# Optimization experiments

Measured on AMD Instinct MI355X. Metric: run time of the kernel, lower is better.

Reference implementation:

```python
import jax, jax.numpy as jnp
import numpy as np

D, B, E, O = 16, 8, 2048, 2048  # delays, batch, pre, post


def setup_inputs() -> dict:
    key = jax.random.key(0)
    k1, k2, k3, k4, k5, k6 = jax.random.split(key, 6)
    # Sparse nonnegative connectivity scaled by wmax (here wmax=1)
    conn = (jax.random.uniform(k1, (E, O)) < 0.2).astype(jnp.float32)
    W = jax.random.uniform(k2, (E, O), dtype=jnp.float32) * conn
    # align_signs: per-presynaptic-neuron sign in {-1,+1}, zeroed where W<=0
    signs_pre = jnp.where(jax.random.uniform(k3, (E,)) < 0.8, 1.0, -1.0)
    signs = jnp.where(W > 0, signs_pre[:, None], 0.0).astype(jnp.float32)
    Xd = (jax.random.uniform(k4, (D, B, E)) < 0.05).astype(jnp.float32)
    # STP module output (before the +1 applied in forward)
    Wshort = 0.1 * jax.random.normal(k5, (D, B, E), dtype=jnp.float32)
    # delaymap: binary routing mask (delay, pre, post)
    delaymap = (jax.random.uniform(k6, (D, E, O)) < 0.3).astype(jnp.float32)
    return {"W": W, "signs": signs, "Xd": Xd, "Wshort": Wshort, "delaymap": delaymap}


def reference(W, signs, Xd, Wshort, delaymap):
    # DeltaSynapse.forward, active, has_STDP=False, has_STP=True:
    #   W_eff = signs * W                      (e, o)
    #   Wshort_mod = shortterm(Xd) + 1         (d, b, e)
    #   I = einsum('eo,dbe,deo,dbe->bo', W_eff, Xd, delaymap, Wshort_mod)
    Weff = signs * W
    I = jnp.einsum('eo,dbe,deo,dbe->bo', Weff, Xd, delaymap, Wshort + 1.0)
    return I
```

## Files before the change

kernel.cpp:

```cpp
#include <hip/hip_runtime.h>
#include <cstdint>
#include <cstddef>

#define DD 16
#define BB 8
#define EE 2048
#define OO 2048
#define NCH 128

__global__ void pack_coeffs(const float* __restrict__ Xd,
                            const float* __restrict__ Ws,
                            float* __restrict__ Cpack,
                            float* __restrict__ out) {
    int i = blockIdx.x * 256 + threadIdx.x;
    if (i < BB * OO) out[i] = 0.0f;
    if (i >= DD * BB * EE) return;
    int e  = i & (EE - 1);
    int db = i >> 11;
    int d  = db >> 3;
    int b  = db & 7;
    float x = Xd[i];
    Cpack[(size_t)e * (DD * BB) + d * BB + b] = x * (Ws[i] + 1.0f);
}

__device__ __forceinline__ void fma4(float4& a, const float4& x, float s) {
    a.x = fmaf(x.x, s, a.x);
    a.y = fmaf(x.y, s, a.y);
    a.z = fmaf(x.z, s, a.z);
    a.w = fmaf(x.w, s, a.w);
}

__global__ __launch_bounds__(256, 4)
void synapse_main(const float* __restrict__ W,
                  const float* __restrict__ S,
                  const float* __restrict__ DM,
                  const float* __restrict__ Cpack,
                  float* __restrict__ out) {
    const int ot    = blockIdx.x;
    const int ch    = blockIdx.y;
    const int wave  = threadIdx.x >> 6;
    const int lane  = threadIdx.x & 63;
    const int o0    = ot * 256 + lane * 4;
    const int ebase = ch * 16 + wave * 4;

    const int q_ln = lane >> 4;
    const int d_ln = lane & 15;
    const float4* crow = reinterpret_cast<const float4*>(
        Cpack + ((size_t)(ebase + q_ln) * (DD * BB)) + d_ln * BB);
    float4 ca = crow[0];
    float4 cb = crow[1];
    bool nz = (ca.x != 0.f) | (ca.y != 0.f) | (ca.z != 0.f) | (ca.w != 0.f) |
              (cb.x != 0.f) | (cb.y != 0.f) | (cb.z != 0.f) | (cb.w != 0.f);
    unsigned long long bal = __ballot(nz);
    unsigned m[4];
#pragma unroll
    for (int q = 0; q < 4; ++q) m[q] = (unsigned)(bal >> (16 * q)) & 0xFFFFu;

    float4 wf[4];
#pragma unroll
    for (int q = 0; q < 4; ++q) {
        float4 w4 = *reinterpret_cast<const float4*>(W + (size_t)(ebase + q) * OO + o0);
        float4 s4 = *reinterpret_cast<const float4*>(S + (size_t)(ebase + q) * OO + o0);
        wf[q].x = w4.x * s4.x; wf[q].y = w4.y * s4.y;
        wf[q].z = w4.z * s4.z; wf[q].w = w4.w * s4.w;
    }

    float4 acc[BB];
#pragma unroll
    for (int b = 0; b < BB; ++b) acc[b] = make_float4(0.f, 0.f, 0.f, 0.f);

    while (m[0] | m[1] | m[2] | m[3]) {
        float4 dmv[4];
        int    dsrc[4];
        unsigned act = 0;
#pragma unroll
        for (int q = 0; q < 4; ++q) {
            if (m[q]) {
                const int d = __builtin_ctz(m[q]);
                m[q] &= (m[q] - 1);
                dsrc[q] = q * 16 + d;
                dmv[q] = *reinterpret_cast<const float4*>(
                    DM + ((size_t)d * EE + (ebase + q)) * OO + o0);
                act |= 1u << q;
            }
        }
#pragma unroll
        for (int q = 0; q < 4; ++q) {
            if (act & (1u << q)) {
                const int sl = dsrc[q];
                float4 dw;
                dw.x = dmv[q].x * wf[q].x; dw.y = dmv[q].y * wf[q].y;
                dw.z = dmv[q].z * wf[q].z; dw.w = dmv[q].w * wf[q].w;
                fma4(acc[0], dw, __shfl(ca.x, sl));
                fma4(acc[1], dw, __shfl(ca.y, sl));
                fma4(acc[2], dw, __shfl(ca.z, sl));
                fma4(acc[3], dw, __shfl(ca.w, sl));
                fma4(acc[4], dw, __shfl(cb.x, sl));
                fma4(acc[5], dw, __shfl(cb.y, sl));
                fma4(acc[6], dw, __shfl(cb.z, sl));
                fma4(acc[7], dw, __shfl(cb.w, sl));
            }
        }
    }

    __shared__ __align__(16) float red[4][4][256];
    const int t = threadIdx.x;
#pragma unroll
    for (int p = 0; p < 2; ++p) {
#pragma unroll
        for (int bb = 0; bb < 4; ++bb)
            *reinterpret_cast<float4*>(&red[wave][bb][lane * 4]) = acc[p * 4 + bb];
        __syncthreads();
#pragma unroll
        for (int bb = 0; bb < 4; ++bb) {
            float s = red[0][bb][t] + red[1][bb][t] +
                      red[2][bb][t] + red[3][bb][t];
            atomicAdd(out + (size_t)(p * 4 + bb) * OO + ot * 256 + t, s);
        }
        __syncthreads();
    }
}

__global__ __launch_bounds__(256, 4)
void synapse_nows(const float* __restrict__ W,
                  const float* __restrict__ S,
                  const float* __restrict__ Xd,
                  const float* __restrict__ Ws,
                  const float* __restrict__ DM,
                  float* __restrict__ out) {
    const int ot    = blockIdx.x;
    const int ch    = blockIdx.y;
    const int wave  = threadIdx.x >> 6;
    const int lane  = threadIdx.x & 63;
    const int o0    = ot * 256 + lane * 4;
    const int ebase = ch * 16 + wave * 4;

    float4 acc[BB];
#pragma unroll
    for (int b = 0; b < BB; ++b) acc[b] = make_float4(0.f, 0.f, 0.f, 0.f);

    for (int ei = 0; ei < 4; ++ei) {
        const int e = ebase + ei;
        float4 w4 = *reinterpret_cast<const float4*>(W + (size_t)e * OO + o0);
        float4 s4 = *reinterpret_cast<const float4*>(S + (size_t)e * OO + o0);
        float4 wf;
        wf.x = w4.x * s4.x; wf.y = w4.y * s4.y;
        wf.z = w4.z * s4.z; wf.w = w4.w * s4.w;

        for (int d = 0; d < DD; ++d) {
            float c[BB];
            bool nz = false;
#pragma unroll
            for (int b = 0; b < BB; ++b) {
                size_t idx = (size_t)(d * BB + b) * EE + e;
                float x = Xd[idx];
                c[b] = x * (Ws[idx] + 1.0f);
                nz |= (c[b] != 0.f);
            }
            if (!nz) continue;
            float4 dm = *reinterpret_cast<const float4*>(
                DM + ((size_t)d * EE + e) * OO + o0);
            float4 dw;
            dw.x = dm.x * wf.x; dw.y = dm.y * wf.y;
            dw.z = dm.z * wf.z; dw.w = dm.w * wf.w;
#pragma unroll
            for (int b = 0; b < BB; ++b) fma4(acc[b], dw, c[b]);
        }
    }

    __shared__ __align__(16) float red[4][4][256];
    const int t = threadIdx.x;
#pragma unroll
    for (int p = 0; p < 2; ++p) {
#pragma unroll
        for (int bb = 0; bb < 4; ++bb)
            *reinterpret_cast<float4*>(&red[wave][bb][lane * 4]) = acc[p * 4 + bb];
        __syncthreads();
#pragma unroll
        for (int bb = 0; bb < 4; ++bb) {
            float s = red[0][bb][t] + red[1][bb][t] +
                      red[2][bb][t] + red[3][bb][t];
            atomicAdd(out + (size_t)(p * 4 + bb) * OO + ot * 256 + t, s);
        }
        __syncthreads();
    }
}

__global__ void zero_out(float* __restrict__ out) {
    int i = blockIdx.x * 256 + threadIdx.x;
    if (i < BB * OO) out[i] = 0.0f;
}

extern "C" void kernel_launch(void* const* d_in, const int* in_sizes, int n_in,
                              void* d_out, int out_size, void* d_ws, size_t ws_size,
                              hipStream_t stream) {
    const float* W  = (const float*)d_in[0];
    const float* S  = (const float*)d_in[1];
    const float* Xd = (const float*)d_in[2];
    const float* Ws = (const float*)d_in[3];
    const float* DM = (const float*)d_in[4];
    float* out = (float*)d_out;

    const size_t packBytes = (size_t)EE * DD * BB * sizeof(float);

    dim3 grid(8, NCH), blk(256);

    if (ws_size >= packBytes) {
        float* Cp = (float*)d_ws;
        pack_coeffs<<<(DD * BB * EE + 255) / 256, 256, 0, stream>>>(Xd, Ws, Cp, out);
        synapse_main<<<grid, blk, 0, stream>>>(W, S, DM, Cp, out);
    } else {
        zero_out<<<(BB * OO + 255) / 256, 256, 0, stream>>>(out);
        synapse_nows<<<grid, blk, 0, stream>>>(W, S, Xd, Ws, DM, out);
    }
}
```

Measured before the change: 349.3 us.

## Compact active (delay, pre) pairs into a global list and stream-partition them

```diff
diff --git a/kernel.cpp b/kernel.cpp
--- a/kernel.cpp
+++ b/kernel.cpp
@@ -6,13 +6,16 @@
 #define BB 8
 #define EE 2048
 #define OO 2048
-#define NCH 128
-
-__global__ void pack_coeffs(const float* __restrict__ Xd,
-                            const float* __restrict__ Ws,
-                            float* __restrict__ Cpack,
-                            float* __restrict__ out) {
+#define MAXP (EE * DD)
+#define NPART 256
+
+__global__ void prep(const float* __restrict__ Xd,
+                     const float* __restrict__ Ws,
+                     float* __restrict__ Cpack,
+                     unsigned* __restrict__ counter,
+                     float* __restrict__ out) {
     int i = blockIdx.x * 256 + threadIdx.x;
+    if (i == 0) *counter = 0;
     if (i < BB * OO) out[i] = 0.0f;
     if (i >= DD * BB * EE) return;
     int e  = i & (EE - 1);
@@ -23,6 +26,49 @@
     Cpack[(size_t)e * (DD * BB) + d * BB + b] = x * (Ws[i] + 1.0f);
 }
 
+__global__ void build_list(const float* __restrict__ Cpack,
+                           unsigned* __restrict__ counter,
+                           uint2* __restrict__ meta,
+                           float4* __restrict__ coef) {
+    const int t = threadIdx.x;
+    const int e = blockIdx.x * 256 + t;
+
+    unsigned msk = 0;
+    const float4* row = reinterpret_cast<const float4*>(Cpack + (size_t)e * (DD * BB));
+    for (int d = 0; d < DD; ++d) {
+        float4 a = row[d * 2];
+        float4 b = row[d * 2 + 1];
+        bool nz = (a.x != 0.f) | (a.y != 0.f) | (a.z != 0.f) | (a.w != 0.f) |
+                  (b.x != 0.f) | (b.y != 0.f) | (b.z != 0.f) | (b.w != 0.f);
+        msk |= (nz ? 1u : 0u) << d;
+    }
+    unsigned cnt = __popc(msk);
+
+    __shared__ unsigned sc[256];
+    __shared__ unsigned gbase;
+    sc[t] = cnt;
+    __syncthreads();
+    for (int off = 1; off < 256; off <<= 1) {
+        unsigned v = (t >= off) ? sc[t - off] : 0;
+        __syncthreads();
+        sc[t] += v;
+        __syncthreads();
+    }
+    if (t == 255) gbase = atomicAdd(counter, sc[255]);
+    __syncthreads();
+
+    unsigned ofs = gbase + sc[t] - cnt;
+    unsigned mm = msk;
+    while (mm) {
+        const int d = __builtin_ctz(mm);
+        mm &= (mm - 1);
+        meta[ofs] = make_uint2((unsigned)(d * EE + e), (unsigned)e);
+        coef[ofs * 2]     = row[d * 2];
+        coef[ofs * 2 + 1] = row[d * 2 + 1];
+        ++ofs;
+    }
+}
+
 __device__ __forceinline__ void fma4(float4& a, const float4& x, float s) {
     a.x = fmaf(x.x, s, a.x);
     a.y = fmaf(x.y, s, a.y);
@@ -30,95 +76,82 @@
     a.w = fmaf(x.w, s, a.w);
 }
 
-__global__ __launch_bounds__(256, 4)
-void synapse_main(const float* __restrict__ W,
-                  const float* __restrict__ S,
-                  const float* __restrict__ DM,
-                  const float* __restrict__ Cpack,
-                  float* __restrict__ out) {
-    const int ot    = blockIdx.x;
-    const int ch    = blockIdx.y;
-    const int wave  = threadIdx.x >> 6;
-    const int lane  = threadIdx.x & 63;
-    const int o0    = ot * 256 + lane * 4;
-    const int ebase = ch * 16 + wave * 4;
-
-    const int q_ln = lane >> 4;
-    const int d_ln = lane & 15;
-    const float4* crow = reinterpret_cast<const float4*>(
-        Cpack + ((size_t)(ebase + q_ln) * (DD * BB)) + d_ln * BB);
-    float4 ca = crow[0];
-    float4 cb = crow[1];
-    bool nz = (ca.x != 0.f) | (ca.y != 0.f) | (ca.z != 0.f) | (ca.w != 0.f) |
-              (cb.x != 0.f) | (cb.y != 0.f) | (cb.z != 0.f) | (cb.w != 0.f);
-    unsigned long long bal = __ballot(nz);
-    unsigned m[4];
-#pragma unroll
-    for (int q = 0; q < 4; ++q) m[q] = (unsigned)(bal >> (16 * q)) & 0xFFFFu;
-
-    float4 wf[4];
-#pragma unroll
-    for (int q = 0; q < 4; ++q) {
-        float4 w4 = *reinterpret_cast<const float4*>(W + (size_t)(ebase + q) * OO + o0);
-        float4 s4 = *reinterpret_cast<const float4*>(S + (size_t)(ebase + q) * OO + o0);
-        wf[q].x = w4.x * s4.x; wf[q].y = w4.y * s4.y;
-        wf[q].z = w4.z * s4.z; wf[q].w = w4.w * s4.w;
-    }
+__global__ __launch_bounds__(256, 2)
+void synapse_stream(const float* __restrict__ W,
+                    const float* __restrict__ S,
+                    const float* __restrict__ DM,
+                    const unsigned* __restrict__ counter,
+                    const uint2* __restrict__ meta,
+                    const float4* __restrict__ coef,
+                    float* __restrict__ out) {
+    const int o0 = blockIdx.y * 1024 + threadIdx.x * 4;
+    const unsigned P = *counter;
+    const int chunk = (int)((P + NPART - 1) / NPART);
+    int p  = blockIdx.x * chunk;
+    int p1 = p + chunk;
+    if (p1 > (int)P) p1 = (int)P;
 
     float4 acc[BB];
 #pragma unroll
     for (int b = 0; b < BB; ++b) acc[b] = make_float4(0.f, 0.f, 0.f, 0.f);
 
-    while (m[0] | m[1] | m[2] | m[3]) {
-        float4 dmv[4];
-        int    dsrc[4];
-        unsigned act = 0;
-#pragma unroll
-        for (int q = 0; q < 4; ++q) {
-            if (m[q]) {
-                const int d = __builtin_ctz(m[q]);
-                m[q] &= (m[q] - 1);
-                dsrc[q] = q * 16 + d;
-                dmv[q] = *reinterpret_cast<const float4*>(
-                    DM + ((size_t)d * EE + (ebase + q)) * OO + o0);
-                act |= 1u << q;
-            }
-        }
-#pragma unroll
-        for (int q = 0; q < 4; ++q) {
-            if (act & (1u << q)) {
-                const int sl = dsrc[q];
-                float4 dw;
-                dw.x = dmv[q].x * wf[q].x; dw.y = dmv[q].y * wf[q].y;
-                dw.z = dmv[q].z * wf[q].z; dw.w = dmv[q].w * wf[q].w;
-                fma4(acc[0], dw, __shfl(ca.x, sl));
-                fma4(acc[1], dw, __shfl(ca.y, sl));
-                fma4(acc[2], dw, __shfl(ca.z, sl));
-                fma4(acc[3], dw, __shfl(ca.w, sl));
-                fma4(acc[4], dw, __shfl(cb.x, sl));
-                fma4(acc[5], dw, __shfl(cb.y, sl));
-                fma4(acc[6], dw, __shfl(cb.z, sl));
-                fma4(acc[7], dw, __shfl(cb.w, sl));
-            }
-        }
-    }
-
-    __shared__ __align__(16) float red[4][4][256];
-    const int t = threadIdx.x;
-#pragma unroll
-    for (int p = 0; p < 2; ++p) {
-#pragma unroll
-        for (int bb = 0; bb < 4; ++bb)
-            *reinterpret_cast<float4*>(&red[wave][bb][lane * 4]) = acc[p * 4 + bb];
-        __syncthreads();
-#pragma unroll
-        for (int bb = 0; bb < 4; ++bb) {
-            float s = red[0][bb][t] + red[1][bb][t] +
-                      red[2][bb][t] + red[3][bb][t];
-            atomicAdd(out + (size_t)(p * 4 + bb) * OO + ot * 256 + t, s);
-        }
-        __syncthreads();
-    }
+    for (; p + 4 <= p1; p += 4) {
+        uint2  mv[4];
+        float4 dm[4], w4[4], s4[4];
+#pragma unroll
+        for (int j = 0; j < 4; ++j) mv[j] = meta[p + j];
+#pragma unroll
+        for (int j = 0; j < 4; ++j) {
+            dm[j] = *reinterpret_cast<const float4*>(DM + (size_t)mv[j].x * OO + o0);
+            w4[j] = *reinterpret_cast<const float4*>(W  + (size_t)mv[j].y * OO + o0);
+            s4[j] = *reinterpret_cast<const float4*>(S  + (size_t)mv[j].y * OO + o0);
+        }
+#pragma unroll
+        for (int j = 0; j < 4; ++j) {
+            float4 c0 = coef[(size_t)(p + j) * 2];
+            float4 c1 = coef[(size_t)(p + j) * 2 + 1];
+            float4 dw;
+            dw.x = dm[j].x * w4[j].x * s4[j].x;
+            dw.y = dm[j].y * w4[j].y * s4[j].y;
+            dw.z = dm[j].z * w4[j].z * s4[j].z;
+            dw.w = dm[j].w * w4[j].w * s4[j].w;
+            fma4(acc[0], dw, c0.x); fma4(acc[1], dw, c0.y);
+            fma4(acc[2], dw, c0.z); fma4(acc[3], dw, c0.w);
+            fma4(acc[4], dw, c1.x); fma4(acc[5], dw, c1.y);
+            fma4(acc[6], dw, c1.z); fma4(acc[7], dw, c1.w);
+        }
+    }
+    for (; p < p1; ++p) {
+        uint2 mv = meta[p];
+        float4 dm = *reinterpret_cast<const float4*>(DM + (size_t)mv.x * OO + o0);
+        float4 w4 = *reinterpret_cast<const float4*>(W  + (size_t)mv.y * OO + o0);
+        float4 s4 = *reinterpret_cast<const float4*>(S  + (size_t)mv.y * OO + o0);
+        float4 c0 = coef[(size_t)p * 2];
+        float4 c1 = coef[(size_t)p * 2 + 1];
+        float4 dw;
+        dw.x = dm.x * w4.x * s4.x;
+        dw.y = dm.y * w4.y * s4.y;
+        dw.z = dm.z * w4.z * s4.z;
+        dw.w = dm.w * w4.w * s4.w;
+        fma4(acc[0], dw, c0.x); fma4(acc[1], dw, c0.y);
+        fma4(acc[2], dw, c0.z); fma4(acc[3], dw, c0.w);
+        fma4(acc[4], dw, c1.x); fma4(acc[5], dw, c1.y);
+        fma4(acc[6], dw, c1.z); fma4(acc[7], dw, c1.w);
+    }
+
+#pragma unroll
+    for (int b = 0; b < BB; ++b) {
+        float* op = out + (size_t)b * OO + o0;
+        atomicAdd(op + 0, acc[b].x);
+        atomicAdd(op + 1, acc[b].y);
+        atomicAdd(op + 2, acc[b].z);
+        atomicAdd(op + 3, acc[b].w);
+    }
+}
+
+__global__ void zero_out(float* __restrict__ out) {
+    int i = blockIdx.x * 256 + threadIdx.x;
+    if (i < BB * OO) out[i] = 0.0f;
 }
 
 __global__ __launch_bounds__(256, 4)
@@ -171,24 +204,19 @@
     __shared__ __align__(16) float red[4][4][256];
     const int t = threadIdx.x;
 #pragma unroll
-    for (int p = 0; p < 2; ++p) {
+    for (int pp = 0; pp < 2; ++pp) {
 #pragma unroll
         for (int bb = 0; bb < 4; ++bb)
-            *reinterpret_cast<float4*>(&red[wave][bb][lane * 4]) = acc[p * 4 + bb];
+            *reinterpret_cast<float4*>(&red[wave][bb][lane * 4]) = acc[pp * 4 + bb];
         __syncthreads();
 #pragma unroll
         for (int bb = 0; bb < 4; ++bb) {
             float s = red[0][bb][t] + red[1][bb][t] +
                       red[2][bb][t] + red[3][bb][t];
-            atomicAdd(out + (size_t)(p * 4 + bb) * OO + ot * 256 + t, s);
-        }
-        __syncthreads();
-    }
-}
-
-__global__ void zero_out(float* __restrict__ out) {
-    int i = blockIdx.x * 256 + threadIdx.x;
-    if (i < BB * OO) out[i] = 0.0f;
+            atomicAdd(out + (size_t)(pp * 4 + bb) * OO + ot * 256 + t, s);
+        }
+        __syncthreads();
+    }
 }
 
 extern "C" void kernel_launch(void* const* d_in, const int* in_sizes, int n_in,
@@ -201,16 +229,24 @@
     const float* DM = (const float*)d_in[4];
     float* out = (float*)d_out;
 
-    const size_t packBytes = (size_t)EE * DD * BB * sizeof(float);
-
-    dim3 grid(8, NCH), blk(256);
-
-    if (ws_size >= packBytes) {
-        float* Cp = (float*)d_ws;
-        pack_coeffs<<<(DD * BB * EE + 255) / 256, 256, 0, stream>>>(Xd, Ws, Cp, out);
-        synapse_main<<<grid, blk, 0, stream>>>(W, S, DM, Cp, out);
+    const size_t cpackBytes = (size_t)EE * DD * BB * sizeof(float);
+    const size_t ctrOff     = cpackBytes;
+    const size_t metaOff    = ctrOff + 256;
+    const size_t coefOff    = metaOff + (size_t)MAXP * sizeof(uint2);
+    const size_t totalWs    = coefOff + (size_t)MAXP * 8 * sizeof(float);
+
+    char* ws = (char*)d_ws;
+
+    if (ws_size >= totalWs) {
+        float*    Cp  = (float*)ws;
+        unsigned* ctr = (unsigned*)(ws + ctrOff);
+        uint2*    mt  = (uint2*)(ws + metaOff);
+        float4*   cf  = (float4*)(ws + coefOff);
+        prep<<<(DD * BB * EE + 255) / 256, 256, 0, stream>>>(Xd, Ws, Cp, ctr, out);
+        build_list<<<EE / 256, 256, 0, stream>>>(Cp, ctr, mt, cf);
+        synapse_stream<<<dim3(NPART, 2), 256, 0, stream>>>(W, S, DM, ctr, mt, cf, out);
     } else {
         zero_out<<<(BB * OO + 255) / 256, 256, 0, stream>>>(out);
-        synapse_nows<<<grid, blk, 0, stream>>>(W, S, Xd, Ws, DM, out);
-    }
-}
+        synapse_nows<<<dim3(8, 128), 256, 0, stream>>>(W, S, Xd, Ws, DM, out);
+    }
+}
```

Result: slower. 433.5 us (+24.1%).
